# Kernel tuning notes

Hardware: AMD Instinct MI355X
Metric: run time of the kernel (lower is better)

The kernel has to match this reference:

```python
import jax, jax.numpy as jnp
from jax import lax
import numpy as np

B, H, W = 8, 36, 100  # stride-8 feature map of 288x800 input
PAD = 4               # ms_ks // 2 for ms_ks = 9
EPS = 1e-5
FC_IN = 5 * (800 // 16) * (288 // 16)  # 4500


def setup_inputs() -> dict:
    key = jax.random.key(0)
    ks = jax.random.split(key, 12)
    r = lambda k, s, sc: jax.random.normal(k, s, jnp.float32) * sc
    return {
        "x": jax.random.normal(ks[0], (B, 512, H, W), jnp.float32),
        "w1a": r(ks[1], (1024, 512, 3, 3), 0.02),
        "bn1_g": jnp.ones(1024, jnp.float32), "bn1_b": jnp.zeros(1024, jnp.float32),
        "bn1_m": jnp.zeros(1024, jnp.float32), "bn1_v": jnp.ones(1024, jnp.float32),
        "w1b": r(ks[2], (128, 1024, 1, 1), 0.03),
        "bn2_g": jnp.ones(128, jnp.float32), "bn2_b": jnp.zeros(128, jnp.float32),
        "bn2_m": jnp.zeros(128, jnp.float32), "bn2_v": jnp.ones(128, jnp.float32),
        "w_ud": r(ks[3], (128, 128, 9), 0.02),
        "w_du": r(ks[4], (128, 128, 9), 0.02),
        "w_lr": r(ks[5], (128, 128, 9), 0.02),
        "w_rl": r(ks[6], (128, 128, 9), 0.02),
        "w2": r(ks[7], (5, 128, 1, 1), 0.05), "b2": jnp.zeros(5, jnp.float32),
        "fc1_w": r(ks[8], (128, FC_IN), 0.02), "fc1_b": jnp.zeros(128, jnp.float32),
        "fc2_w": r(ks[9], (4, 128), 0.05), "fc2_b": jnp.zeros(4, jnp.float32),
    }


def bn(x, g, b, m, v):
    s = (g / jnp.sqrt(v + EPS))
    return x * s[None, :, None, None] + (b - m * s)[None, :, None, None]


def conv2d(x, w, padding, dilation=(1, 1)):
    return lax.conv_general_dilated(x, w, (1, 1), padding, rhs_dilation=dilation,
                                    dimension_numbers=("NCHW", "OIHW", "NCHW"))


def conv1d(x, w):  # x [B,C,L], w [O,I,K]
    return lax.conv_general_dilated(x, w, (1,), [(PAD, PAD)],
                                    dimension_numbers=("NCH", "OIH", "NCH"))


def message_pass(x, w, axis, reverse):
    # x [B,C,H,W]; scan over `axis`, 1D conv along the other spatial dim
    xs = jnp.moveaxis(x, axis, 0)  # [L, B, C, other]
    if reverse:
        xs = xs[::-1]

    def step(prev, cur):
        new = cur + jax.nn.relu(conv1d(prev, w))
        return new, new

    first = xs[0]
    _, rest = lax.scan(step, first, xs[1:])
    out = jnp.concatenate([first[None], rest], axis=0)
    if reverse:
        out = out[::-1]
    return jnp.moveaxis(out, 0, axis)


def upsample_bilinear_ac(x, scale):
    # align_corners=True bilinear, NCHW
    b, c, h, w = x.shape
    ho, wo = h * scale, w * scale

    def grid(n_in, n_out):
        pos = jnp.arange(n_out, dtype=x.dtype) * ((n_in - 1) / (n_out - 1))
        i0 = jnp.clip(jnp.floor(pos).astype(jnp.int32), 0, n_in - 2)
        return i0, pos - i0.astype(x.dtype)

    i0, fh = grid(h, ho)
    j0, fw = grid(w, wo)
    xh = x[:, :, i0, :] * (1 - fh)[None, None, :, None] + x[:, :, i0 + 1, :] * fh[None, None, :, None]
    return xh[:, :, :, j0] * (1 - fw)[None, None, None, :] + xh[:, :, :, j0 + 1] * fw[None, None, None, :]


def reference(x, w1a, bn1_g, bn1_b, bn1_m, bn1_v, w1b, bn2_g, bn2_b, bn2_m, bn2_v,
              w_ud, w_du, w_lr, w_rl, w2, b2, fc1_w, fc1_b, fc2_w, fc2_b):
    # layer1: dilated 3x3 (pad=4, dil=4) -> BN -> ReLU -> 1x1 -> BN -> ReLU
    h = jax.nn.relu(bn(conv2d(x, w1a, [(4, 4), (4, 4)], dilation=(4, 4)), bn1_g, bn1_b, bn1_m, bn1_v))
    h = jax.nn.relu(bn(conv2d(h, w1b, [(0, 0), (0, 0)]), bn2_g, bn2_b, bn2_m, bn2_v))
    # message passing: up-down, down-up (vertical), left-right, right-left (horizontal)
    h = message_pass(h, w_ud, axis=2, reverse=False)
    h = message_pass(h, w_du, axis=2, reverse=True)
    h = message_pass(h, w_lr, axis=3, reverse=False)
    h = message_pass(h, w_rl, axis=3, reverse=True)
    # layer2 (Dropout2d is identity at eval): 1x1 conv -> 5 channels
    h = conv2d(h, w2, [(0, 0), (0, 0)]) + b2[None, :, None, None]
    seg_pred = upsample_bilinear_ac(h, 8)  # [B,5,288,800]
    # layer3: softmax over channels, then AvgPool2d(2,2)
    p = jax.nn.softmax(h, axis=1)
    b_, c_, hh, ww = p.shape
    p = p.reshape(b_, c_, hh // 2, 2, ww // 2, 2).mean(axis=(3, 5))
    # fc: flatten -> 128 -> ReLU -> 4 -> Sigmoid
    f = p.reshape(b_, -1)
    f = jax.nn.relu(f @ fc1_w.T + fc1_b)
    exist_pred = jax.nn.sigmoid(f @ fc2_w.T + fc2_b)
    return seg_pred, exist_pred
```

## Files before the change

kernel.cpp:

```cpp
#include <hip/hip_runtime.h>
#include <hip/hip_bf16.h>
#include <stdint.h>

typedef __bf16 bf16;
typedef bf16 bf16x8 __attribute__((ext_vector_type(8)));
typedef bf16 bf16x4 __attribute__((ext_vector_type(4)));
typedef float f32x4 __attribute__((ext_vector_type(4)));
typedef unsigned long long u64;

#define NB 8
#define NH 36
#define NW 100
#define YS 44
#define XSZ 108
#define PIX 28800

#define AS1 __attribute__((address_space(1)))
#define AS3 __attribute__((address_space(3)))

__device__ __forceinline__ void g2l16(const bf16* g, bf16* l) {
    __builtin_amdgcn_global_load_lds((const AS1 void*)g, (AS3 void*)l, 16, 0, 0);
}

static constexpr size_t OFF_XP = 0;
static constexpr size_t SZ_XP  = (size_t)NB*YS*XSZ*512*2;
static constexpr size_t OFF_HP = OFF_XP + SZ_XP;
static constexpr size_t SZ_HP  = (size_t)NB*YS*XSZ*128*2;
static constexpr size_t OFF_A1 = OFF_HP + SZ_HP;
static constexpr size_t SZ_A1  = (size_t)1024*4608*2;
static constexpr size_t OFF_A2 = OFF_A1 + SZ_A1;
static constexpr size_t SZ_A2  = (size_t)128*1024*2;
static constexpr size_t OFF_AW = OFF_A2 + SZ_A2;
static constexpr size_t SZ_AW  = (size_t)4*9*128*128*2;
static constexpr size_t OFF_H1 = OFF_AW + SZ_AW;
static constexpr size_t SZ_H1  = (size_t)PIX*1024*2;
static constexpr size_t OFF_S1 = OFF_H1 + SZ_H1;
static constexpr size_t OFF_T1 = OFF_S1 + 4096;
static constexpr size_t OFF_S2 = OFF_T1 + 4096;
static constexpr size_t OFF_T2 = OFF_S2 + 512;
static constexpr size_t OFF_H5 = OFF_T2 + 512;
static constexpr size_t SZ_H5  = (size_t)NB*5*3600*4;
static constexpr size_t OFF_P  = OFF_H5 + SZ_H5;
static constexpr size_t OFF_F  = OFF_P + SZ_H5;
static constexpr size_t OFF_G  = OFF_F + 144128;
static constexpr size_t OFF_BAR = OFF_G + 4096;

__global__ __launch_bounds__(256) void zero_k(uint4* __restrict__ p, int n) {
    int i = blockIdx.x * 256 + threadIdx.x;
    if (i < n) p[i] = uint4{0u, 0u, 0u, 0u};
}

__global__ __launch_bounds__(256) void prep_x(const float* __restrict__ x, bf16* __restrict__ xp) {
    int bid = blockIdx.x;
    int xc = bid & 3;  int r = bid >> 2;
    int cc = r & 15;   r >>= 4;
    int yo = r % 36;   int b = r / 36;
    int ci0 = cc * 32, xo0 = xc * 32;
    int wdt = 100 - xo0; if (wdt > 32) wdt = 32;
    __shared__ bf16 T[32 * 33];
    int t = threadIdx.x;
    int cl = t >> 5, xl = t & 31;
    if (xl < wdt) {
#pragma unroll
        for (int i = 0; i < 4; i++) {
            int ci = ci0 + cl + 8 * i;
            T[(cl + 8 * i) * 33 + xl] = (bf16)x[((size_t)(b * 512 + ci) * 36 + yo) * 100 + xo0 + xl];
        }
    }
    __syncthreads();
    if (t < 128) {
        int xo2 = t >> 2, oct = t & 3;
        if (xo2 < wdt) {
            bf16x8 vv;
#pragma unroll
            for (int j = 0; j < 8; j++) vv[j] = T[(oct * 8 + j) * 33 + xo2];
            *(bf16x8*)(xp + ((size_t)((b * YS + yo + 4) * XSZ) + xo0 + xo2 + 4) * 512 + ci0 + oct * 8) = vv;
        }
    }
}

__global__ __launch_bounds__(256) void prep_w1a(const float* __restrict__ w, bf16* __restrict__ A) {
    int co = blockIdx.x;
    __shared__ bf16 Wl[4608];
    const float* src = w + (size_t)co * 4608;
    for (int v = threadIdx.x; v < 4608; v += 256) Wl[v] = (bf16)src[v];
    __syncthreads();
    bf16* dst = A + (size_t)co * 4608;
    for (int v = threadIdx.x; v < 4608; v += 256) {
        int rr = v >> 9, ci = v & 511;
        dst[v] = Wl[ci * 9 + rr];
    }
}

__global__ __launch_bounds__(256) void prep_w1b(const float* __restrict__ w, bf16* __restrict__ A) {
    int i = blockIdx.x * 256 + threadIdx.x;
    if (i < 131072) A[i] = (bf16)w[i];
}

__global__ __launch_bounds__(256) void prep_msg(const float* __restrict__ w0, const float* __restrict__ w1,
                                                const float* __restrict__ w2m, const float* __restrict__ w3,
                                                bf16* __restrict__ Aw) {
    int idx = blockIdx.x * 256 + threadIdx.x;
    if (idx >= 4 * 147456) return;
    int w = idx / 147456, r = idx % 147456;
    int t9 = r / 16384, r2 = r % 16384;
    int co = r2 >> 7, ci = r2 & 127;
    const float* s = (w == 0) ? w0 : (w == 1) ? w1 : (w == 2) ? w2m : w3;
    Aw[idx] = (bf16)s[(co * 128 + ci) * 9 + t9];
}

__global__ __launch_bounds__(256) void prep_bn(const float* g1, const float* b1, const float* m1, const float* v1,
                                               const float* g2, const float* b2i, const float* m2, const float* v2,
                                               float* s1, float* t1, float* s2, float* t2,
                                               unsigned* bar) {
    int i = blockIdx.x * 256 + threadIdx.x;
    if (i < 1024) {
        float s = g1[i] / sqrtf(v1[i] + 1e-5f);
        s1[i] = s; t1[i] = b1[i] - m1[i] * s;
    } else if (i < 1152) {
        int c = i - 1024;
        float s = g2[c] / sqrtf(v2[c] + 1e-5f);
        s2[c] = s; t2[c] = b2i[c] - m2[c] * s;
    } else if (i < 1160) {
        bar[i - 1152] = 0u;
    }
}

__device__ __forceinline__ void c1_koff(int ch, int& k0, int& xoff) {
    int ky = ch / 48, rem = ch - ky * 48;
    int kx = rem >> 4, c0 = (rem & 15) << 5;
    k0 = (ky * 3 + kx) * 512 + c0;
    xoff = (ky * XSZ + kx) * 2048 + c0;
}

__device__ __forceinline__ bf16x8 lds_frag(const bf16* S, int row, int q) {
    return *(const bf16x8*)(S + row * 32 + (((q ^ (row >> 1)) & 3) * 8));
}

__global__ __launch_bounds__(256) void conv1_gemm(const bf16* __restrict__ A, const bf16* __restrict__ xp,
                                                  const float* __restrict__ s1, const float* __restrict__ t1,
                                                  bf16* __restrict__ h1) {
    __shared__ __align__(16) bf16 SH[17408];
    bf16* As = SH;
    bf16* Bs = SH + 4096;
    const int t = threadIdx.x;
    const int pt = blockIdx.x, ct = blockIdx.y;
    const int co0 = ct * 128, p0 = pt * 128;
    const int wid = t >> 6, lane = t & 63;

    int aOff[2], bOff[2], ldsOff[2];
#pragma unroll
    for (int j = 0; j < 2; j++) {
        int p = wid * 128 + j * 64 + lane;
        int row = p >> 2;
        int oc = (p & 3) ^ ((p >> 3) & 3);
        aOff[j] = (co0 + row) * 4608 + oc * 8;
        int px = p0 + row;
        int b = px / 3600, rr = px % 3600;
        int y = rr / 100, xx = rr % 100;
        bOff[j] = ((b * YS + y) * XSZ + xx) * 512 + oc * 8;
        ldsOff[j] = (wid * 128 + j * 64) * 8;
    }

    const int mbase = (wid & 1) * 64, nbase = (wid >> 1) * 64;
    const int l15 = lane & 15, q = lane >> 4;

    f32x4 acc[4][4];
#pragma unroll
    for (int i = 0; i < 4; i++)
#pragma unroll
        for (int j = 0; j < 4; j++) acc[i][j] = f32x4{0.f, 0.f, 0.f, 0.f};

    for (int ch = 0; ch < 144; ch++) {
        int k0, xoff;
        c1_koff(ch, k0, xoff);
        __syncthreads();
#pragma unroll
        for (int j = 0; j < 2; j++) {
            g2l16(A + aOff[j] + k0, As + ldsOff[j]);
            g2l16(xp + bOff[j] + xoff, Bs + ldsOff[j]);
        }
        __syncthreads();
        bf16x8 af[4], bfv[4];
#pragma unroll
        for (int mt = 0; mt < 4; mt++) af[mt] = lds_frag(As, mbase + mt * 16 + l15, q);
#pragma unroll
        for (int nt = 0; nt < 4; nt++) bfv[nt] = lds_frag(Bs, nbase + nt * 16 + l15, q);
#pragma unroll
        for (int mt = 0; mt < 4; mt++)
#pragma unroll
            for (int nt = 0; nt < 4; nt++)
                acc[mt][nt] = __builtin_amdgcn_mfma_f32_16x16x32_bf16(af[mt], bfv[nt], acc[mt][nt], 0, 0, 0);
    }

    __syncthreads();
#pragma unroll
    for (int mt = 0; mt < 4; mt++) {
        int co = co0 + mbase + mt * 16 + q * 4;
        f32x4 sc = *(const f32x4*)(s1 + co);
        f32x4 tc = *(const f32x4*)(t1 + co);
#pragma unroll
        for (int nt = 0; nt < 4; nt++) {
            int pxl = nbase + nt * 16 + l15;
            bf16x4 o;
#pragma unroll
            for (int r = 0; r < 4; r++) {
                float v = acc[mt][nt][r] * sc[r] + tc[r];
                o[r] = (bf16)(v > 0.f ? v : 0.f);
            }
            *(bf16x4*)(SH + pxl * 136 + mbase + mt * 16 + q * 4) = o;
        }
    }
    __syncthreads();
#pragma unroll
    for (int i = 0; i < 8; i++) {
        int v = t + 256 * i;
        int pxl = v >> 4, c16 = v & 15;
        *(uint4*)(h1 + (size_t)(p0 + pxl) * 1024 + co0 + c16 * 8) = *(const uint4*)(SH + pxl * 136 + c16 * 8);
    }
}

__global__ __launch_bounds__(256) void conv2_gemm(const bf16* __restrict__ A2, const bf16* __restrict__ h1,
                                                  const float* __restrict__ s2, const float* __restrict__ t2,
                                                  bf16* __restrict__ hp) {
    __shared__ __align__(16) bf16 SH[17408];
    bf16* As = SH;
    bf16* Bs = SH + 4096;
    const int t = threadIdx.x;
    const int p0 = blockIdx.x * 128;
    const int wid = t >> 6, lane = t & 63;

    int aOff[2], bOff[2], ldsOff[2];
#pragma unroll
    for (int j = 0; j < 2; j++) {
        int p = wid * 128 + j * 64 + lane;
        int row = p >> 2;
        int oc = (p & 3) ^ ((p >> 3) & 3);
        aOff[j] = row * 1024 + oc * 8;
        bOff[j] = (p0 + row) * 1024 + oc * 8;
        ldsOff[j] = (wid * 128 + j * 64) * 8;
    }
    const int mbase = (wid & 1) * 64, nbase = (wid >> 1) * 64;
    const int l15 = lane & 15, q = lane >> 4;

    f32x4 acc[4][4];
#pragma unroll
    for (int i = 0; i < 4; i++)
#pragma unroll
        for (int j = 0; j < 4; j++) acc[i][j] = f32x4{0.f, 0.f, 0.f, 0.f};

    for (int ch = 0; ch < 32; ch++) {
        int k0 = ch * 32;
        __syncthreads();
#pragma unroll
        for (int j = 0; j < 2; j++) {
            g2l16(A2 + aOff[j] + k0, As + ldsOff[j]);
            g2l16(h1 + bOff[j] + k0, Bs + ldsOff[j]);
        }
        __syncthreads();
        bf16x8 af[4], bfv[4];
#pragma unroll
        for (int mt = 0; mt < 4; mt++) af[mt] = lds_frag(As, mbase + mt * 16 + l15, q);
#pragma unroll
        for (int nt = 0; nt < 4; nt++) bfv[nt] = lds_frag(Bs, nbase + nt * 16 + l15, q);
#pragma unroll
        for (int mt = 0; mt < 4; mt++)
#pragma unroll
            for (int nt = 0; nt < 4; nt++)
                acc[mt][nt] = __builtin_amdgcn_mfma_f32_16x16x32_bf16(af[mt], bfv[nt], acc[mt][nt], 0, 0, 0);
    }

    __syncthreads();
#pragma unroll
    for (int mt = 0; mt < 4; mt++) {
        int co = mbase + mt * 16 + q * 4;
        f32x4 sc = *(const f32x4*)(s2 + co);
        f32x4 tc = *(const f32x4*)(t2 + co);
#pragma unroll
        for (int nt = 0; nt < 4; nt++) {
            int pxl = nbase + nt * 16 + l15;
            bf16x4 o;
#pragma unroll
            for (int r = 0; r < 4; r++) {
                float v = acc[mt][nt][r] * sc[r] + tc[r];
                o[r] = (bf16)(v > 0.f ? v : 0.f);
            }
            *(bf16x4*)(SH + pxl * 136 + co) = o;
        }
    }
    __syncthreads();
#pragma unroll
    for (int i = 0; i < 8; i++) {
        int v = t + 256 * i;
        int pxl = v >> 4, c16 = v & 15;
        int p = p0 + pxl;
        int b = p / 3600, rr = p % 3600;
        int y = rr / 100, xx = rr % 100;
        *(uint4*)(hp + (size_t)((b * YS + y + 4) * XSZ + xx + 4) * 128 + c16 * 8) = *(const uint4*)(SH + pxl * 136 + c16 * 8);
    }
}

__device__ __forceinline__ bf16x8 awfrag2(const bf16* __restrict__ Aw, int ch, int cs, int l15, int q) {
    int t9 = ch >> 2, c0 = (ch & 3) << 5;
    return *(const bf16x8*)(Aw + (size_t)((t9 * 128 + cs * 16 + l15) << 7) + c0 + q * 8);
}

template <int AX, int RV>
__device__ void phase1cu(const bf16* __restrict__ Aw, bf16* __restrict__ hpb,
                         bf16*& bp, bf16*& bn) {
    constexpr int STEPS = (AX == 2) ? NH : NW;
    constexpr int NLIM  = (AX == 2) ? NW : NH;
    constexpr int NT    = (AX == 2) ? 7 : 3;
    const int t = threadIdx.x, wid = t >> 6, lane = t & 63, l15 = lane & 15, q = lane >> 4;

    bf16x8 a[36];
#pragma unroll
    for (int ch = 0; ch < 36; ch++) a[ch] = awfrag2(Aw, ch, wid, l15, q);

    const int co = wid * 16 + q * 4;
    const int pos0 = RV ? (STEPS - 1) : 0;

    if (AX == 2) {
        const bf16* src = hpb + (size_t)(pos0 + 4) * XSZ * 128;
        for (int v = t; v < XSZ * 16; v += 512) {
            int px = v >> 4, c = (v & 15) * 8;
            *(uint4*)(bp + px * 136 + c) = *(const uint4*)(src + px * 128 + c);
        }
    } else {
        for (int v = t; v < 2 * 16 * 17; v += 512) {
            int bsel = v >= 272;
            int r2 = v - bsel * 272;
            bf16* dst = bsel ? bn : bp;
            *(uint4*)(dst + (40 + (r2 / 17)) * 136 + (r2 % 17) * 8) = uint4{0u, 0u, 0u, 0u};
        }
        const bf16* src = hpb + (size_t)(pos0 + 4) * 128;
        for (int v = t; v < 40 * 16; v += 512) {
            int ys = v >> 4, c = (v & 15) * 8;
            *(uint4*)(bp + ys * 136 + c) = *(const uint4*)(src + (size_t)ys * XSZ * 128 + c);
        }
    }
    __syncthreads();

    for (int s = 1; s < STEPS; s++) {
        const int pos = RV ? (STEPS - 1 - s) : s;

        int goff[NT];
        u64 curv[NT];
#pragma unroll
        for (int i = 0; i < NT; i++) {
            int n = i * 16 + l15;
            goff[i] = (AX == 2) ? ((pos + 4) * XSZ + n + 4) * 128 + co
                                : ((n + 4) * XSZ + pos + 4) * 128 + co;
            curv[i] = 0;
            if (n < NLIM) curv[i] = *(const u64*)(hpb + goff[i]);
        }

        f32x4 acc[NT];
#pragma unroll
        for (int i = 0; i < NT; i++) acc[i] = f32x4{0.f, 0.f, 0.f, 0.f};
#pragma unroll
        for (int ch = 0; ch < 36; ch++) {
            const int t9 = ch >> 2, c0 = (ch & 3) << 5;
            const bf16* base = bp + (l15 + t9) * 136 + c0 + q * 8;
#pragma unroll
            for (int i = 0; i < NT; i++) {
                bf16x8 bfv = *(const bf16x8*)(base + i * 16 * 136);
                acc[i] = __builtin_amdgcn_mfma_f32_16x16x32_bf16(a[ch], bfv, acc[i], 0, 0, 0);
            }
        }

#pragma unroll
        for (int i = 0; i < NT; i++) {
            int n = i * 16 + l15;
            if (n < NLIM) {
                bf16x4 cur = *(bf16x4*)&curv[i];
                bf16x4 o;
#pragma unroll
                for (int r = 0; r < 4; r++) {
                    float v = acc[i][r];
                    v = v > 0.f ? v : 0.f;
                    o[r] = (bf16)((float)cur[r] + v);
                }
                *(u64*)(hpb + goff[i]) = *(u64*)&o;
                *(u64*)(bn + (n + 4) * 136 + co) = *(u64*)&o;
            }
        }
        __syncthreads();
        bf16* tmp = bp; bp = bn; bn = tmp;
    }
}

__global__ __launch_bounds__(512, 2) void msg_fused(const bf16* __restrict__ Aw, bf16* __restrict__ hp) {
    __shared__ __align__(16) bf16 BUF[2][120 * 136];
    const int batch = blockIdx.x;
    bf16* hpb = hp + (size_t)batch * YS * XSZ * 128;
    for (int v = threadIdx.x; v < 2 * 120 * 17; v += 512)
        ((uint4*)BUF)[v] = uint4{0u, 0u, 0u, 0u};
    __syncthreads();
    bf16* bp = BUF[0];
    bf16* bn = BUF[1];
    phase1cu<2, 0>(Aw + 0 * 147456, hpb, bp, bn);
    phase1cu<2, 1>(Aw + 1 * 147456, hpb, bp, bn);
    phase1cu<3, 0>(Aw + 2 * 147456, hpb, bp, bn);
    phase1cu<3, 1>(Aw + 3 * 147456, hpb, bp, bn);
}

__global__ __launch_bounds__(256) void conv3_softmax(const bf16* __restrict__ hp, const float* __restrict__ w2,
                                                     const float* __restrict__ b2, float* __restrict__ h5,
                                                     float* __restrict__ Pp) {
    int idx = blockIdx.x * 256 + threadIdx.x;
    if (idx >= PIX) return;
    int b = idx / 3600, rr = idx % 3600;
    int y = rr / 100, xx = rr % 100;
    const bf16* src = hp + ((size_t)(b * YS + y + 4) * XSZ + xx + 4) * 128;
    float a[5] = {b2[0], b2[1], b2[2], b2[3], b2[4]};
    for (int c8 = 0; c8 < 128; c8 += 8) {
        bf16x8 hv = *(const bf16x8*)(src + c8);
#pragma unroll
        for (int j = 0; j < 8; j++) {
            float hf = (float)hv[j];
            int c = c8 + j;
#pragma unroll
            for (int o = 0; o < 5; o++) a[o] += hf * w2[o * 128 + c];
        }
    }
    float mx = a[0];
#pragma unroll
    for (int o = 1; o < 5; o++) mx = a[o] > mx ? a[o] : mx;
    float e[5], sum = 0.f;
#pragma unroll
    for (int o = 0; o < 5; o++) { e[o] = expf(a[o] - mx); sum += e[o]; }
    float inv = 1.f / sum;
#pragma unroll
    for (int o = 0; o < 5; o++) {
        h5[(size_t)(b * 5 + o) * 3600 + rr] = a[o];
        Pp[(size_t)(b * 5 + o) * 3600 + rr] = e[o] * inv;
    }
}

__global__ __launch_bounds__(256) void pool_k(const float* __restrict__ Pp, float* __restrict__ F) {
    int idx = blockIdx.x * 256 + threadIdx.x;
    if (idx >= 36000) return;
    int xxp = idx % 50, r = idx / 50;
    int yyp = r % 18, bj = r / 18;
    int b = bj / 5, j = bj % 5;
    const float* Pb = Pp + (size_t)bj * 3600;
    float v = 0.25f * (Pb[(2 * yyp) * 100 + 2 * xxp] + Pb[(2 * yyp) * 100 + 2 * xxp + 1] +
                       Pb[(2 * yyp + 1) * 100 + 2 * xxp] + Pb[(2 * yyp + 1) * 100 + 2 * xxp + 1]);
    F[(size_t)b * 4500 + j * 900 + yyp * 50 + xxp] = v;
}

__global__ __launch_bounds__(64) void fc1_k(const float* __restrict__ F, const float* __restrict__ w,
                                            const float* __restrict__ bias, float* __restrict__ G) {
    int co = blockIdx.x;
    int lane = threadIdx.x;
    const float* wr = w + (size_t)co * 4500;
    float a[8] = {0.f, 0.f, 0.f, 0.f, 0.f, 0.f, 0.f, 0.f};
    for (int k = lane; k < 4500; k += 64) {
        float wv = wr[k];
#pragma unroll
        for (int b = 0; b < 8; b++) a[b] += wv * F[b * 4500 + k];
    }
#pragma unroll
    for (int b = 0; b < 8; b++) {
        float r = a[b];
        for (int off = 32; off; off >>= 1) r += __shfl_down(r, off);
        if (lane == 0) {
            float v = r + bias[co];
            G[b * 128 + co] = v > 0.f ? v : 0.f;
        }
    }
}

__global__ __launch_bounds__(64) void fc2_k(const float* __restrict__ G, const float* __restrict__ w,
                                            const float* __restrict__ bias, float* __restrict__ out) {
    int t = threadIdx.x;
    if (t >= 32) return;
    int b = t >> 2, j = t & 3;
    float a = bias[j];
    for (int c = 0; c < 128; c++) a += G[b * 128 + c] * w[j * 128 + c];
    out[9216000 + b * 4 + j] = 1.f / (1.f + expf(-a));
}

__global__ __launch_bounds__(256) void upsample_k(const float* __restrict__ h5, float* __restrict__ out) {
    int idx = blockIdx.x * 256 + threadIdx.x;
    if (idx >= 2304000) return;
    int xq = idx % 200, r = idx / 200;
    int yo = r % 288, bj = r / 288;
    const float* src = h5 + (size_t)bj * 3600;
    float py = yo * (35.0f / 287.0f);
    int i0 = (int)py; if (i0 > 34) i0 = 34;
    float fh = py - (float)i0;
    const float* r0 = src + i0 * 100;
    const float* r1 = r0 + 100;
    float4 o;
    float res[4];
#pragma unroll
    for (int e = 0; e < 4; e++) {
        int xo = xq * 4 + e;
        float px = xo * (99.0f / 799.0f);
        int j0 = (int)px; if (j0 > 98) j0 = 98;
        float fw = px - (float)j0;
        float aa = r0[j0] * (1.f - fh) + r1[j0] * fh;
        float bb = r0[j0 + 1] * (1.f - fh) + r1[j0 + 1] * fh;
        res[e] = aa * (1.f - fw) + bb * fw;
    }
    o.x = res[0]; o.y = res[1]; o.z = res[2]; o.w = res[3];
    *(float4*)(out + (size_t)idx * 4) = o;
}

extern "C" void kernel_launch(void* const* d_in, const int* in_sizes, int n_in,
                              void* d_out, int out_size, void* d_ws, size_t ws_size,
                              hipStream_t stream) {
    (void)in_sizes; (void)n_in; (void)out_size; (void)ws_size;
    const float* x    = (const float*)d_in[0];
    const float* w1a  = (const float*)d_in[1];
    const float* bn1g = (const float*)d_in[2];
    const float* bn1b = (const float*)d_in[3];
    const float* bn1m = (const float*)d_in[4];
    const float* bn1v = (const float*)d_in[5];
    const float* w1b  = (const float*)d_in[6];
    const float* bn2g = (const float*)d_in[7];
    const float* bn2b = (const float*)d_in[8];
    const float* bn2m = (const float*)d_in[9];
    const float* bn2v = (const float*)d_in[10];
    const float* wud  = (const float*)d_in[11];
    const float* wdu  = (const float*)d_in[12];
    const float* wlr  = (const float*)d_in[13];
    const float* wrl  = (const float*)d_in[14];
    const float* w2   = (const float*)d_in[15];
    const float* b2   = (const float*)d_in[16];
    const float* fc1w = (const float*)d_in[17];
    const float* fc1b = (const float*)d_in[18];
    const float* fc2w = (const float*)d_in[19];
    const float* fc2b = (const float*)d_in[20];
    float* out = (float*)d_out;
    char* ws = (char*)d_ws;
    bf16* xp = (bf16*)(ws + OFF_XP);
    bf16* hp = (bf16*)(ws + OFF_HP);
    bf16* A1 = (bf16*)(ws + OFF_A1);
    bf16* A2 = (bf16*)(ws + OFF_A2);
    bf16* Aw = (bf16*)(ws + OFF_AW);
    bf16* h1 = (bf16*)(ws + OFF_H1);
    float* s1 = (float*)(ws + OFF_S1);
    float* t1 = (float*)(ws + OFF_T1);
    float* s2 = (float*)(ws + OFF_S2);
    float* t2 = (float*)(ws + OFF_T2);
    float* h5 = (float*)(ws + OFF_H5);
    float* Pp = (float*)(ws + OFF_P);
    float* Ff = (float*)(ws + OFF_F);
    float* Gg = (float*)(ws + OFF_G);
    unsigned* bar = (unsigned*)(ws + OFF_BAR);

    int nzero = (int)((SZ_XP + SZ_HP) / 16);
    zero_k<<<(nzero + 255) / 256, 256, 0, stream>>>((uint4*)ws, nzero);
    prep_x<<<18432, 256, 0, stream>>>(x, xp);
    prep_w1a<<<1024, 256, 0, stream>>>(w1a, A1);
    prep_w1b<<<512, 256, 0, stream>>>(w1b, A2);
    prep_msg<<<2304, 256, 0, stream>>>(wud, wdu, wlr, wrl, Aw);
    prep_bn<<<5, 256, 0, stream>>>(bn1g, bn1b, bn1m, bn1v, bn2g, bn2b, bn2m, bn2v, s1, t1, s2, t2, bar);

    conv1_gemm<<<dim3(225, 8), 256, 0, stream>>>(A1, xp, s1, t1, h1);
    conv2_gemm<<<225, 256, 0, stream>>>(A2, h1, s2, t2, hp);

    msg_fused<<<8, 512, 0, stream>>>(Aw, hp);

    conv3_softmax<<<113, 256, 0, stream>>>(hp, w2, b2, h5, Pp);
    pool_k<<<141, 256, 0, stream>>>(Pp, Ff);
    fc1_k<<<128, 64, 0, stream>>>(Ff, fc1w, fc1b, Gg);
    fc2_k<<<1, 64, 0, stream>>>(Gg, fc2w, fc2b, out);
    upsample_k<<<9000, 256, 0, stream>>>(h5, out);
}
```

Baseline: 1.951 ms.

## Reuse loaded B fragments across conv taps via DPP lane shifts in message passing

The 9-tap 1D conv in the message-passing scan used to load a fresh B fragment from LDS for each tap and tile. It now loads two adjacent 16-row fragments per tile and builds each shifted tap window in registers with DPP row shift/rotate ops, reusing fragments between consecutive tiles. The aim is to cut LDS read traffic in the latency-bound sequential scan, at the cost of extra VALU DPP instructions and register pressure. The LDS buffer is enlarged to 128 rows so the extra prefetched fragment can be read safely.

```diff
diff --git a/kernel.cpp b/kernel.cpp
--- a/kernel.cpp
+++ b/kernel.cpp
@@ -20,6 +20,31 @@
 
 __device__ __forceinline__ void g2l16(const bf16* g, bf16* l) {
     __builtin_amdgcn_global_load_lds((const AS1 void*)g, (AS3 void*)l, 16, 0, 0);
+}
+
+__device__ __forceinline__ bf16x8 dpp_shl1(bf16x8 oldv, bf16x8 srcv) {
+    union { bf16x8 v; int i[4]; } o, s, d;
+    o.v = oldv; s.v = srcv;
+#pragma unroll
+    for (int k = 0; k < 4; k++)
+        d.i[k] = __builtin_amdgcn_update_dpp(o.i[k], s.i[k], 0x101, 0xF, 0xF, false);
+    return d.v;
+}
+__device__ __forceinline__ bf16x8 dpp_rol1(bf16x8 srcv) {
+    union { bf16x8 v; int i[4]; } s, d;
+    s.v = srcv;
+#pragma unroll
+    for (int k = 0; k < 4; k++)
+        d.i[k] = __builtin_amdgcn_update_dpp(s.i[k], s.i[k], 0x12F, 0xF, 0xF, false);
+    return d.v;
+}
+__device__ __forceinline__ bf16x8 dpp_ror8(bf16x8 srcv) {
+    union { bf16x8 v; int i[4]; } s, d;
+    s.v = srcv;
+#pragma unroll
+    for (int k = 0; k < 4; k++)
+        d.i[k] = __builtin_amdgcn_update_dpp(s.i[k], s.i[k], 0x128, 0xF, 0xF, false);
+    return d.v;
 }
 
 static constexpr size_t OFF_XP = 0;
@@ -305,6 +330,40 @@
     return *(const bf16x8*)(Aw + (size_t)((t9 * 128 + cs * 16 + l15) << 7) + c0 + q * 8);
 }
 
+template <int I, int NT>
+__device__ __forceinline__ void tile_step(const bf16x8* __restrict__ a, bf16x8* Wf, bf16x8* Xf,
+                                          f32x4& acc, const bf16* __restrict__ bp, int lo) {
+#pragma unroll
+    for (int j = 0; j < 4; j++)
+        acc = __builtin_amdgcn_mfma_f32_16x16x32_bf16(a[j], Wf[j], acc, 0, 0, 0);
+#pragma unroll
+    for (int j = 0; j < 4; j++) Xf[j] = dpp_rol1(Xf[j]);
+#pragma unroll
+    for (int j = 0; j < 4; j++) {
+        Wf[j] = dpp_shl1(Xf[j], Wf[j]);
+        acc = __builtin_amdgcn_mfma_f32_16x16x32_bf16(a[4 + j], Wf[j], acc, 0, 0, 0);
+        Xf[j] = dpp_rol1(Xf[j]);
+    }
+#pragma unroll
+    for (int t9 = 2; t9 < 9; t9++) {
+#pragma unroll
+        for (int j = 0; j < 4; j++) {
+            Wf[j] = dpp_shl1(Xf[j], Wf[j]);
+            acc = __builtin_amdgcn_mfma_f32_16x16x32_bf16(a[t9 * 4 + j], Wf[j], acc, 0, 0, 0);
+            if (t9 < 8) Xf[j] = dpp_rol1(Xf[j]);
+        }
+    }
+    if constexpr (I + 2 <= NT) {
+#pragma unroll
+        for (int j = 0; j < 4; j++)
+            Wf[j] = *(const bf16x8*)(bp + (I + 2) * 16 * 136 + lo + j * 32);
+    }
+    if constexpr (I + 1 < NT) {
+#pragma unroll
+        for (int j = 0; j < 4; j++) Xf[j] = dpp_ror8(Xf[j]);
+    }
+}
+
 template <int AX, int RV>
 __device__ void phase1cu(const bf16* __restrict__ Aw, bf16* __restrict__ hpb,
                          bf16*& bp, bf16*& bn) {
@@ -341,6 +400,8 @@
     }
     __syncthreads();
 
+    const int lo = l15 * 136 + q * 8;
+
     for (int s = 1; s < STEPS; s++) {
         const int pos = RV ? (STEPS - 1 - s) : s;
 
@@ -355,19 +416,24 @@
             if (n < NLIM) curv[i] = *(const u64*)(hpb + goff[i]);
         }
 
+        bf16x8 W[4], X[4];
+#pragma unroll
+        for (int j = 0; j < 4; j++) {
+            W[j] = *(const bf16x8*)(bp + lo + j * 32);
+            X[j] = *(const bf16x8*)(bp + 16 * 136 + lo + j * 32);
+        }
+
         f32x4 acc[NT];
 #pragma unroll
         for (int i = 0; i < NT; i++) acc[i] = f32x4{0.f, 0.f, 0.f, 0.f};
-#pragma unroll
-        for (int ch = 0; ch < 36; ch++) {
-            const int t9 = ch >> 2, c0 = (ch & 3) << 5;
-            const bf16* base = bp + (l15 + t9) * 136 + c0 + q * 8;
-#pragma unroll
-            for (int i = 0; i < NT; i++) {
-                bf16x8 bfv = *(const bf16x8*)(base + i * 16 * 136);
-                acc[i] = __builtin_amdgcn_mfma_f32_16x16x32_bf16(a[ch], bfv, acc[i], 0, 0, 0);
-            }
-        }
+
+        tile_step<0, NT>(a, W, X, acc[0], bp, lo);
+        if constexpr (NT > 1) tile_step<1, NT>(a, X, W, acc[1], bp, lo);
+        if constexpr (NT > 2) tile_step<2, NT>(a, W, X, acc[2], bp, lo);
+        if constexpr (NT > 3) tile_step<3, NT>(a, X, W, acc[3], bp, lo);
+        if constexpr (NT > 4) tile_step<4, NT>(a, W, X, acc[4], bp, lo);
+        if constexpr (NT > 5) tile_step<5, NT>(a, X, W, acc[5], bp, lo);
+        if constexpr (NT > 6) tile_step<6, NT>(a, W, X, acc[6], bp, lo);
 
 #pragma unroll
         for (int i = 0; i < NT; i++) {
@@ -391,10 +457,10 @@
 }
 
 __global__ __launch_bounds__(512, 2) void msg_fused(const bf16* __restrict__ Aw, bf16* __restrict__ hp) {
-    __shared__ __align__(16) bf16 BUF[2][120 * 136];
+    __shared__ __align__(16) bf16 BUF[2][128 * 136];
     const int batch = blockIdx.x;
     bf16* hpb = hp + (size_t)batch * YS * XSZ * 128;
-    for (int v = threadIdx.x; v < 2 * 120 * 17; v += 512)
+    for (int v = threadIdx.x; v < 2 * 128 * 17; v += 512)
         ((uint4*)BUF)[v] = uint4{0u, 0u, 0u, 0u};
     __syncthreads();
     bf16* bp = BUF[0];
```

New measurement: 2.668 ms. 36.8% more time.

## Rewrite message-passing scan with 32x32 MFMA, split-K waves and swizzled LDS

Applied to the files above, without the earlier changes.

Rewrites the fused message-passing kernel to use 32x32x16 bf16 MFMA instead of 16x16x32. Each wave now owns a 32-channel output slice and half of the K range, and the two halves are combined through an fp32 scratch area in LDS with an extra barrier per step. The weight prep is changed to emit fragments in the new lane order. The activation buffers drop the padded stride for an XOR-swizzled 256-byte row layout to avoid bank conflicts. The aim is to cut per-step latency on the serial scan, at the cost of extra LDS traffic and synchronisation, and the block now uses 128KB of LDS.

```diff
diff --git a/kernel.cpp b/kernel.cpp
--- a/kernel.cpp
+++ b/kernel.cpp
@@ -6,6 +6,7 @@
 typedef bf16 bf16x8 __attribute__((ext_vector_type(8)));
 typedef bf16 bf16x4 __attribute__((ext_vector_type(4)));
 typedef float f32x4 __attribute__((ext_vector_type(4)));
+typedef float f32x16 __attribute__((ext_vector_type(16)));
 typedef unsigned long long u64;
 
 #define NB 8
@@ -102,9 +103,13 @@
                                                 bf16* __restrict__ Aw) {
     int idx = blockIdx.x * 256 + threadIdx.x;
     if (idx >= 4 * 147456) return;
-    int w = idx / 147456, r = idx % 147456;
-    int t9 = r / 16384, r2 = r % 16384;
-    int co = r2 >> 7, ci = r2 & 127;
+    int w = idx / 147456, rem = idx % 147456;
+    int t9 = rem / 16384, r2 = rem % 16384;
+    int kchunk = r2 / 2048, r3 = r2 % 2048;
+    int slice = r3 / 512, r4 = r3 % 512;
+    int lane = r4 >> 3, r = r4 & 7;
+    int co = slice * 32 + (lane & 31);
+    int ci = kchunk * 16 + (lane >> 5) * 8 + r;
     const float* s = (w == 0) ? w0 : (w == 1) ? w1 : (w == 2) ? w2m : w3;
     Aw[idx] = (bf16)s[(co * 128 + ci) * 9 + t9];
 }
@@ -300,43 +305,43 @@
     }
 }
 
-__device__ __forceinline__ bf16x8 awfrag2(const bf16* __restrict__ Aw, int ch, int cs, int l15, int q) {
-    int t9 = ch >> 2, c0 = (ch & 3) << 5;
-    return *(const bf16x8*)(Aw + (size_t)((t9 * 128 + cs * 16 + l15) << 7) + c0 + q * 8);
-}
-
 template <int AX, int RV>
-__device__ void phase1cu(const bf16* __restrict__ Aw, bf16* __restrict__ hpb,
-                         bf16*& bp, bf16*& bn) {
+__device__ void phase32(const bf16* __restrict__ Aw, bf16* __restrict__ hpb,
+                        bf16*& bp, bf16*& bn, float* __restrict__ SCR) {
     constexpr int STEPS = (AX == 2) ? NH : NW;
     constexpr int NLIM  = (AX == 2) ? NW : NH;
-    constexpr int NT    = (AX == 2) ? 7 : 3;
-    const int t = threadIdx.x, wid = t >> 6, lane = t & 63, l15 = lane & 15, q = lane >> 4;
-
-    bf16x8 a[36];
-#pragma unroll
-    for (int ch = 0; ch < 36; ch++) a[ch] = awfrag2(Aw, ch, wid, l15, q);
-
-    const int co = wid * 16 + q * 4;
+    constexpr int NT2   = (AX == 2) ? 4 : 2;
+    const int t = threadIdx.x, wid = t >> 6, l = t & 63, l31 = l & 31, lg = l >> 5;
+    const int slice = wid & 3, khalf = wid >> 2;
+
+    bf16x8 aw[9][4];
+#pragma unroll
+    for (int t9 = 0; t9 < 9; t9++)
+#pragma unroll
+        for (int kc = 0; kc < 4; kc++)
+            aw[t9][kc] = *(const bf16x8*)(Aw + (size_t)((((t9 * 8 + (khalf * 4 + kc)) * 4 + slice) << 9) + l * 8));
+
     const int pos0 = RV ? (STEPS - 1) : 0;
 
     if (AX == 2) {
         const bf16* src = hpb + (size_t)(pos0 + 4) * XSZ * 128;
         for (int v = t; v < XSZ * 16; v += 512) {
-            int px = v >> 4, c = (v & 15) * 8;
-            *(uint4*)(bp + px * 136 + c) = *(const uint4*)(src + px * 128 + c);
+            int px = v >> 4, c16 = v & 15;
+            *(uint4*)((char*)bp + px * 256 + (((c16 ^ (px & 7)) << 4))) =
+                *(const uint4*)(src + px * 128 + c16 * 8);
         }
     } else {
-        for (int v = t; v < 2 * 16 * 17; v += 512) {
-            int bsel = v >= 272;
-            int r2 = v - bsel * 272;
+        for (int v = t; v < 2 * 8 * 16; v += 512) {
+            int bsel = v >= 128;
+            int r2 = v - bsel * 128;
             bf16* dst = bsel ? bn : bp;
-            *(uint4*)(dst + (40 + (r2 / 17)) * 136 + (r2 % 17) * 8) = uint4{0u, 0u, 0u, 0u};
+            *(uint4*)((char*)dst + (40 + (r2 >> 4)) * 256 + ((r2 & 15) << 4)) = uint4{0u, 0u, 0u, 0u};
         }
         const bf16* src = hpb + (size_t)(pos0 + 4) * 128;
         for (int v = t; v < 40 * 16; v += 512) {
-            int ys = v >> 4, c = (v & 15) * 8;
-            *(uint4*)(bp + ys * 136 + c) = *(const uint4*)(src + (size_t)ys * XSZ * 128 + c);
+            int ys = v >> 4, c16 = v & 15;
+            *(uint4*)((char*)bp + ys * 256 + (((c16 ^ (ys & 7)) << 4))) =
+                *(const uint4*)(src + (size_t)ys * XSZ * 128 + c16 * 8);
         }
     }
     __syncthreads();
@@ -344,65 +349,98 @@
     for (int s = 1; s < STEPS; s++) {
         const int pos = RV ? (STEPS - 1 - s) : s;
 
-        int goff[NT];
-        u64 curv[NT];
-#pragma unroll
-        for (int i = 0; i < NT; i++) {
-            int n = i * 16 + l15;
-            goff[i] = (AX == 2) ? ((pos + 4) * XSZ + n + 4) * 128 + co
-                                : ((n + 4) * XSZ + pos + 4) * 128 + co;
-            curv[i] = 0;
-            if (n < NLIM) curv[i] = *(const u64*)(hpb + goff[i]);
-        }
-
-        f32x4 acc[NT];
-#pragma unroll
-        for (int i = 0; i < NT; i++) acc[i] = f32x4{0.f, 0.f, 0.f, 0.f};
-#pragma unroll
-        for (int ch = 0; ch < 36; ch++) {
-            const int t9 = ch >> 2, c0 = (ch & 3) << 5;
-            const bf16* base = bp + (l15 + t9) * 136 + c0 + q * 8;
-#pragma unroll
-            for (int i = 0; i < NT; i++) {
-                bf16x8 bfv = *(const bf16x8*)(base + i * 16 * 136);
-                acc[i] = __builtin_amdgcn_mfma_f32_16x16x32_bf16(a[ch], bfv, acc[i], 0, 0, 0);
+        f32x16 acc[NT2];
+#pragma unroll
+        for (int i = 0; i < NT2; i++)
+#pragma unroll
+            for (int c = 0; c < 16; c++) acc[i][c] = 0.f;
+
+        const char* bpB = (const char*)bp;
+#pragma unroll
+        for (int t9 = 0; t9 < 9; t9++) {
+            const int row0 = l31 + t9;
+            const int base = row0 * 256;
+            const int x = row0 & 7;
+#pragma unroll
+            for (int kc = 0; kc < 4; kc++) {
+                const int kb = (khalf * 4 + kc) * 2 + lg;
+                const char* p = bpB + base + (((kb ^ x) << 4));
+#pragma unroll
+                for (int i = 0; i < NT2; i++) {
+                    bf16x8 bv = *(const bf16x8*)(p + i * 8192);
+                    acc[i] = __builtin_amdgcn_mfma_f32_32x32x16_bf16(aw[t9][kc], bv, acc[i], 0, 0, 0);
+                }
             }
         }
 
-#pragma unroll
-        for (int i = 0; i < NT; i++) {
-            int n = i * 16 + l15;
-            if (n < NLIM) {
-                bf16x4 cur = *(bf16x4*)&curv[i];
-                bf16x4 o;
-#pragma unroll
-                for (int r = 0; r < 4; r++) {
-                    float v = acc[i][r];
-                    v = v > 0.f ? v : 0.f;
-                    o[r] = (bf16)((float)cur[r] + v);
-                }
-                *(u64*)(hpb + goff[i]) = *(u64*)&o;
-                *(u64*)(bn + (n + 4) * 136 + co) = *(u64*)&o;
-            }
-        }
+        u64 curv[2][4];
+#define SCRW(J) do { float* _s = SCR + ((slice * NT2 + (J)) << 10) + l * 4;                      \
+        f32x4 _v0 = {acc[J][0], acc[J][1], acc[J][2], acc[J][3]};   *(f32x4*)(_s)       = _v0;  \
+        f32x4 _v1 = {acc[J][4], acc[J][5], acc[J][6], acc[J][7]};   *(f32x4*)(_s + 256) = _v1;  \
+        f32x4 _v2 = {acc[J][8], acc[J][9], acc[J][10], acc[J][11]}; *(f32x4*)(_s + 512) = _v2;  \
+        f32x4 _v3 = {acc[J][12], acc[J][13], acc[J][14], acc[J][15]}; *(f32x4*)(_s + 768) = _v3; } while (0)
+#define CURP(J, S) do { int _n = (J) * 32 + l31; bool _ok = _n < NLIM;                           \
+        _Pragma("unroll") for (int g = 0; g < 4; g++) {                                         \
+            int _co = slice * 32 + g * 8 + lg * 4;                                              \
+            int _go = (AX == 2) ? ((pos + 4) * XSZ + _n + 4) * 128 + _co                        \
+                                : ((_n + 4) * XSZ + pos + 4) * 128 + _co;                       \
+            curv[S][g] = _ok ? *(const u64*)(hpb + _go) : 0ull; } } while (0)
+#define EPIL(J, S) do { int _n = (J) * 32 + l31;                                                \
+        if (_n < NLIM) {                                                                        \
+            const float* _s = SCR + ((slice * NT2 + (J)) << 10) + l * 4;                        \
+            int _rb = (_n + 4) * 256, _x7 = (_n + 4) & 7;                                       \
+            _Pragma("unroll") for (int g = 0; g < 4; g++) {                                     \
+                int _co = slice * 32 + g * 8 + lg * 4;                                          \
+                int _go = (AX == 2) ? ((pos + 4) * XSZ + _n + 4) * 128 + _co                    \
+                                    : ((_n + 4) * XSZ + pos + 4) * 128 + _co;                   \
+                f32x4 part = *(const f32x4*)(_s + g * 256);                                     \
+                bf16x4 cur = *(bf16x4*)&curv[S][g]; bf16x4 o;                                   \
+                _Pragma("unroll") for (int c = 0; c < 4; c++) {                                 \
+                    float v = acc[J][4 * g + c] + part[c];                                      \
+                    v = v > 0.f ? v : 0.f;                                                      \
+                    o[c] = (bf16)((float)cur[c] + v); }                                         \
+                *(u64*)(hpb + _go) = *(u64*)&o;                                                 \
+                *(u64*)((char*)bn + _rb + ((((slice * 4 + g) ^ _x7) << 4)) + lg * 8) = *(u64*)&o; } } } while (0)
+
+        if (NT2 == 4) {
+            if (khalf == 0) { SCRW(2); SCRW(3); CURP(0, 0); CURP(1, 1); }
+            else            { SCRW(0); SCRW(1); CURP(2, 0); CURP(3, 1); }
+        } else {
+            if (khalf == 0) { SCRW(1); CURP(0, 0); }
+            else            { SCRW(0); CURP(1, 0); }
+        }
+        __syncthreads();
+        if (NT2 == 4) {
+            if (khalf == 0) { EPIL(0, 0); EPIL(1, 1); }
+            else            { EPIL(2, 0); EPIL(3, 1); }
+        } else {
+            if (khalf == 0) { EPIL(0, 0); }
+            else            { EPIL(1, 0); }
+        }
+#undef SCRW
+#undef CURP
+#undef EPIL
         __syncthreads();
         bf16* tmp = bp; bp = bn; bn = tmp;
     }
 }
 
 __global__ __launch_bounds__(512, 2) void msg_fused(const bf16* __restrict__ Aw, bf16* __restrict__ hp) {
-    __shared__ __align__(16) bf16 BUF[2][120 * 136];
+    __shared__ __align__(16) char LDSM[131072];
+    bf16* b0 = (bf16*)LDSM;
+    bf16* b1 = (bf16*)(LDSM + 32768);
+    float* SCR = (float*)(LDSM + 65536);
     const int batch = blockIdx.x;
     bf16* hpb = hp + (size_t)batch * YS * XSZ * 128;
-    for (int v = threadIdx.x; v < 2 * 120 * 17; v += 512)
-        ((uint4*)BUF)[v] = uint4{0u, 0u, 0u, 0u};
-    __syncthreads();
-    bf16* bp = BUF[0];
-    bf16* bn = BUF[1];
-    phase1cu<2, 0>(Aw + 0 * 147456, hpb, bp, bn);
-    phase1cu<2, 1>(Aw + 1 * 147456, hpb, bp, bn);
-    phase1cu<3, 0>(Aw + 2 * 147456, hpb, bp, bn);
-    phase1cu<3, 1>(Aw + 3 * 147456, hpb, bp, bn);
+    for (int v = threadIdx.x; v < 4096; v += 512)
+        ((uint4*)LDSM)[v] = uint4{0u, 0u, 0u, 0u};
+    __syncthreads();
+    bf16* bp = b0;
+    bf16* bn = b1;
+    phase32<2, 0>(Aw + 0 * 147456, hpb, bp, bn, SCR);
+    phase32<2, 1>(Aw + 1 * 147456, hpb, bp, bn, SCR);
+    phase32<3, 0>(Aw + 2 * 147456, hpb, bp, bn, SCR);
+    phase32<3, 1>(Aw + 3 * 147456, hpb, bp, bn, SCR);
 }
 
 __global__ __launch_bounds__(256) void conv3_softmax(const bf16* __restrict__ hp, const float* __restrict__ w2,
```

Measured after the change: 2.789 ms. +43.0%, slower.
